# Kernel tuning notes

Measured on AMD Instinct MI355X. Metric: run time of the kernel, lower is better.

## Reference

```python
import jax, jax.numpy as jnp
import numpy as np

# --- batched state-vector quantum circuit sim: AngleEmbedding(RY) + BasicEntanglerLayers(RX + ring CNOT) ---

def _ry(state, theta, wire, n):
    # per-sample RY(theta) on `wire`; state: (B,) + (2,)*n complex
    ax = wire + 1
    c = jnp.cos(0.5 * theta).reshape((-1,) + (1,) * (n - 1)).astype(state.dtype)
    s = jnp.sin(0.5 * theta).reshape((-1,) + (1,) * (n - 1)).astype(state.dtype)
    s0 = jnp.take(state, 0, axis=ax)
    s1 = jnp.take(state, 1, axis=ax)
    return jnp.stack([c * s0 - s * s1, s * s0 + c * s1], axis=ax)

def _rx(state, theta, wire, n):
    # scalar RX(theta) on `wire` (shared weight across batch)
    ax = wire + 1
    c = jnp.cos(0.5 * theta).astype(state.dtype)
    s = (-1j * jnp.sin(0.5 * theta)).astype(state.dtype)
    s0 = jnp.take(state, 0, axis=ax)
    s1 = jnp.take(state, 1, axis=ax)
    return jnp.stack([c * s0 + s * s1, s * s0 + c * s1], axis=ax)

def _cnot(state, ctrl, tgt):
    ax_c = ctrl + 1
    s0 = jnp.take(state, 0, axis=ax_c)
    s1 = jnp.take(state, 1, axis=ax_c)
    ax_t = tgt + 1 if tgt < ctrl else tgt  # target axis index after removing ctrl axis
    s1 = jnp.flip(s1, axis=ax_t)
    return jnp.stack([s0, s1], axis=ax_c)

def _circuit(x_qin, qweights):
    # x_qin: (Bn, n) angles; qweights: (L, n)
    Bn, n = x_qin.shape
    state = jnp.zeros((Bn,) + (2,) * n, jnp.complex64)
    state = state.at[(slice(None),) + (0,) * n].set(1.0)
    for w in range(n):  # AngleEmbedding, rotation='Y'
        state = _ry(state, x_qin[:, w], w, n)
    for l in range(qweights.shape[0]):  # BasicEntanglerLayers
        for w in range(n):
            state = _rx(state, qweights[l, w], w, n)
        for w in range(n):
            state = _cnot(state, w, (w + 1) % n)
    probs = jnp.real(state * jnp.conj(state))
    outs = []
    for w in range(n):  # <Z_w> = P(bit_w=0) - P(bit_w=1)
        axes = tuple(a for a in range(1, n + 1) if a != w + 1)
        p = probs.sum(axis=axes)  # (Bn, 2)
        outs.append(p[:, 0] - p[:, 1])
    return jnp.stack(outs, axis=-1).astype(jnp.float32)


def setup_inputs() -> dict:
    key = jax.random.key(0)
    ks = jax.random.split(key, 9)
    B, N, H, NQ, L = 16, 1024, 256, 8, 2
    x = jax.random.normal(ks[0], (B, N, H), jnp.float32)
    norm_adj = jax.random.uniform(ks[1], (N, N), jnp.float32) / N
    Wg = jax.random.normal(ks[2], (H, H), jnp.float32) * 0.02
    bg = jax.random.normal(ks[3], (H,), jnp.float32) * 0.02
    Wpre = jax.random.normal(ks[4], (NQ, H), jnp.float32) * 0.05
    bpre = jax.random.normal(ks[5], (NQ,), jnp.float32) * 0.02
    qweights = jax.random.uniform(ks[6], (L, NQ), jnp.float32) * (2.0 * np.pi)
    Wpost = jax.random.normal(ks[7], (H, NQ), jnp.float32) * 0.1
    bpost = jax.random.normal(ks[8], (H,), jnp.float32) * 0.02
    return {"x": x, "norm_adj": norm_adj, "Wg": Wg, "bg": bg, "Wpre": Wpre,
            "bpre": bpre, "qweights": qweights, "Wpost": Wpost, "bpost": bpost}


def reference(x, norm_adj, Wg, bg, Wpre, bpre, qweights, Wpost, bpost):
    # GCN aggregation + GELU(Linear)  (dropout is identity in eval mode)
    x_agg = jnp.einsum('ij,bjh->bih', norm_adj, x)
    x_agg = jax.nn.gelu(x_agg @ Wg.T + bg, approximate=False)
    B, N, H = x_agg.shape
    x_flat = x_agg.reshape(B * N, H).astype(jnp.float32)
    x_qin = jnp.tanh(x_flat @ Wpre.T + bpre) * np.pi
    q_out = _circuit(x_qin, qweights)          # (B*N, n_qubits)
    out = (q_out @ Wpost.T + bpost).reshape(B, N, H)
    return out
```

## Files before the change

kernel.cpp:

```cpp
#include <hip/hip_runtime.h>
#include <math.h>

typedef __attribute__((ext_vector_type(8))) short bf16x8;
typedef _Float16 f16x8 __attribute__((ext_vector_type(8)));
typedef __attribute__((ext_vector_type(4))) float f32x4;

#define PI_F 3.14159265358979323846f

__device__ __forceinline__ unsigned short f2bf(float f) {
  unsigned int u = __float_as_uint(f);
  u += 0x7FFFu + ((u >> 16) & 1u);
  return (unsigned short)(u >> 16);
}

__device__ __forceinline__ float bf2f(unsigned short u) {
  return __uint_as_float(((unsigned int)u) << 16);
}

__device__ __forceinline__ void async_ld16(const unsigned short* g, unsigned short* l) {
  __builtin_amdgcn_global_load_lds(
      (const __attribute__((address_space(1))) void*)g,
      (__attribute__((address_space(3))) void*)l,
      16, 0, 0);
}

__device__ __forceinline__ float fast_erf(float x) {
  float a = fabsf(x);
  float t = 1.0f / fmaf(0.3275911f, a, 1.0f);
  float p = t * fmaf(t, fmaf(t, fmaf(t, fmaf(t, 1.061405429f, -1.453152027f),
                                     1.421413741f), -0.284496736f), 0.254829592f);
  float e = __expf(-a * a);
  float r = 1.0f - p * e;
  return copysignf(r, x);
}

__device__ __forceinline__ float fast_tanh(float a) {
  float e = __expf(2.0f * a);
  return 1.0f - 2.0f / (e + 1.0f);
}

template<int ML, int MR>
__device__ __forceinline__ void apply_rx(float re[4], float im[4], float c, float s) {
  float pr[4], pi[4];
  #pragma unroll
  for (int r = 0; r < 4; r++) {
    float vr = re[r ^ MR], vi = im[r ^ MR];
    if (ML) { vr = __shfl_xor(vr, ML, 64); vi = __shfl_xor(vi, ML, 64); }
    pr[r] = vr; pi[r] = vi;
  }
  #pragma unroll
  for (int r = 0; r < 4; r++) {
    re[r] = fmaf(c, re[r],  s * pi[r]);
    im[r] = fmaf(c, im[r], -s * pr[r]);
  }
}

__device__ __forceinline__ void fold_reduce8(float v[8], int L) {
  #pragma unroll
  for (int step = 0; step < 3; step++) {
    int d = 1 << step;
    int half = 4 >> step;
    bool hi = (L & d) != 0;
    #pragma unroll
    for (int w = 0; w < half; w++) {
      float send = hi ? v[w] : v[w + half];
      float recv = __shfl_xor(send, d, 64);
      v[w] = (hi ? v[w + half] : v[w]) + recv;
    }
  }
  v[0] += __shfl_xor(v[0], 8, 64);
  v[0] += __shfl_xor(v[0], 16, 64);
  v[0] += __shfl_xor(v[0], 32, 64);
}

__global__ __launch_bounds__(256)
void prep_kernel(const float* __restrict__ adj, unsigned short* __restrict__ adj_bf,
                 const float* __restrict__ Wg, unsigned short* __restrict__ Wg_bf,
                 const float* __restrict__ qw, unsigned short* __restrict__ Uri,
                 const float* __restrict__ Wpost, _Float16* __restrict__ Gt,
                 const float* __restrict__ x, unsigned short* __restrict__ xT) {
  __shared__ float smem[1056];
  int bid = blockIdx.x, t = threadIdx.x;
  if (bid < 1024) {
    int i = bid * 256 + t;
    float4 v = ((const float4*)adj)[i];
    ushort4 o; o.x = f2bf(v.x); o.y = f2bf(v.y); o.z = f2bf(v.z); o.w = f2bf(v.w);
    ((ushort4*)adj_bf)[i] = o;
  } else if (bid < 1088) {
    int i = (bid - 1024) * 256 + t;
    float4 v = ((const float4*)Wg)[i];
    ushort4 o; o.x = f2bf(v.x); o.y = f2bf(v.y); o.z = f2bf(v.z); o.w = f2bf(v.w);
    ((ushort4*)Wg_bf)[i] = o;
  } else if (bid < 1152) {
    if (t < 16) { smem[t] = cosf(0.5f * qw[t]); smem[16 + t] = sinf(0.5f * qw[t]); }
    __syncthreads();
    int wv = t >> 6, L = t & 63;
    int k = (bid - 1088) * 4 + wv;
    float re[4], im[4];
    #pragma unroll
    for (int r = 0; r < 4; r++) { re[r] = (r * 64 + L == k) ? 1.f : 0.f; im[r] = 0.f; }
    apply_rx<1, 0>(re, im, smem[0], smem[16]);
    apply_rx<2, 0>(re, im, smem[1], smem[17]);
    apply_rx<4, 0>(re, im, smem[2], smem[18]);
    apply_rx<8, 0>(re, im, smem[3], smem[19]);
    apply_rx<16, 0>(re, im, smem[4], smem[20]);
    apply_rx<32, 0>(re, im, smem[5], smem[21]);
    apply_rx<0, 1>(re, im, smem[6], smem[22]);
    apply_rx<0, 2>(re, im, smem[7], smem[23]);
    apply_rx<3, 0>(re, im, smem[8], smem[24]);
    apply_rx<6, 0>(re, im, smem[9], smem[25]);
    apply_rx<12, 0>(re, im, smem[10], smem[26]);
    apply_rx<24, 0>(re, im, smem[11], smem[27]);
    apply_rx<48, 0>(re, im, smem[12], smem[28]);
    apply_rx<32, 1>(re, im, smem[13], smem[29]);
    apply_rx<0, 3>(re, im, smem[14], smem[30]);
    apply_rx<3, 2>(re, im, smem[15], smem[31]);
    const int M[8] = {0xAB, 0xFD, 0xFA, 0xF5, 0xEA, 0xD5, 0xAA, 0x55};
    #pragma unroll
    for (int r = 0; r < 4; r++) {
      int n = 0;
      #pragma unroll
      for (int w = 0; w < 8; w++) {
        int bit = (__popc(L & (M[w] & 63)) ^ __popc((r << 6) & M[w])) & 1;
        n |= bit << w;
      }
      int row_re = ((n >> 4) << 5) + (n & 15);
      Uri[(size_t)row_re * 256 + k] = f2bf(re[r]);
      Uri[(size_t)(row_re + 16) * 256 + k] = f2bf(im[r]);
    }
  } else if (bid < 1168) {
    int tid = (bid - 1152) * 256 + t;
    int h = tid >> 4;
    int n0 = (tid & 15) << 4;
    float wv8[8];
    #pragma unroll
    for (int w = 0; w < 8; w++) wv8[w] = Wpost[h * 8 + w];
    #pragma unroll
    for (int j = 0; j < 16; j++) {
      int n = n0 + j;
      float sum = 0.f;
      #pragma unroll
      for (int w = 0; w < 8; w++) sum += ((n >> w) & 1) ? -wv8[w] : wv8[w];
      Gt[h * 256 + n] = (_Float16)sum;
    }
  } else {
    int tb = bid - 1168;
    int jt = tb & 31, ht = (tb >> 5) & 7, bb = tb >> 8;
    int tx = t & 31, ty = t >> 5;
    const float* xb = x + (size_t)bb * 1024 * 256;
    #pragma unroll
    for (int i = 0; i < 4; i++) {
      int j = jt * 32 + ty + i * 8;
      smem[(ty + i * 8) * 33 + tx] = xb[(size_t)j * 256 + ht * 32 + tx];
    }
    __syncthreads();
    unsigned short* xTb = xT + (size_t)bb * 256 * 1024;
    #pragma unroll
    for (int i = 0; i < 4; i++) {
      int h = ht * 32 + ty + i * 8;
      xTb[(size_t)h * 1024 + jt * 32 + tx] = f2bf(smem[tx * 33 + ty + i * 8]);
    }
  }
}

__global__ __launch_bounds__(256)
void gemm1_kernel(const unsigned short* __restrict__ A,
                  const unsigned short* __restrict__ Bt,
                  unsigned short* __restrict__ C,
                  int K, int tilesN, int ldC) {
  __shared__ unsigned short As[2 * 128 * 32];
  __shared__ unsigned short Bs[2 * 64 * 32];
  int rr  = blockIdx.x;
  int im  = rr / tilesN;
  int in_ = rr % tilesN;
  const unsigned short* Ab  = A  + (long long)im * 128 * K;
  const unsigned short* Btb = Bt + (long long)in_ * 64 * K;

  int t = threadIdx.x;
  int wv = t >> 6, lane = t & 63;
  int wm = wv >> 1, wn = wv & 1;
  int l15 = lane & 15, quad = lane >> 4;

  f32x4 acc[4][2] = {};

  for (int kk = 0; kk < K; kk += 64) {
    __syncthreads();
    #pragma unroll
    for (int kb = 0; kb < 2; kb++) {
      #pragma unroll
      for (int q = 0; q < 2; q++) {
        int ch = q * 256 + t;
        async_ld16(Ab + (long long)(ch >> 2) * K + kk + kb * 32 + (ch & 3) * 8,
                   &As[kb * 4096 + ch * 8]);
      }
      {
        int ch = t;
        async_ld16(Btb + (long long)(ch >> 2) * K + kk + kb * 32 + (ch & 3) * 8,
                   &Bs[kb * 2048 + ch * 8]);
      }
    }
    __syncthreads();
    #pragma unroll
    for (int kb = 0; kb < 2; kb++) {
      bf16x8 af[4], bfr[2];
      #pragma unroll
      for (int mt = 0; mt < 4; mt++)
        af[mt] = *(const bf16x8*)&As[kb * 4096 + (wm * 64 + mt * 16 + l15) * 32 + quad * 8];
      #pragma unroll
      for (int nt = 0; nt < 2; nt++)
        bfr[nt] = *(const bf16x8*)&Bs[kb * 2048 + (wn * 32 + nt * 16 + l15) * 32 + quad * 8];
      #pragma unroll
      for (int mt = 0; mt < 4; mt++)
        #pragma unroll
        for (int nt = 0; nt < 2; nt++)
          acc[mt][nt] = __builtin_amdgcn_mfma_f32_16x16x32_bf16(af[mt], bfr[nt], acc[mt][nt], 0, 0, 0);
    }
  }

  int n0 = in_ * 64;
  #pragma unroll
  for (int mt = 0; mt < 4; mt++) {
    #pragma unroll
    for (int nt = 0; nt < 2; nt++) {
      int colg = n0 + wn * 32 + nt * 16 + l15;
      #pragma unroll
      for (int r = 0; r < 4; r++) {
        int rowg = im * 128 + wm * 64 + mt * 16 + quad * 4 + r;
        C[(size_t)rowg * ldC + colg] = f2bf(acc[mt][nt][r]);
      }
    }
  }
}

__global__ __launch_bounds__(256)
void qfused_kernel(const unsigned short* __restrict__ xagg,
                   const unsigned short* __restrict__ Wg,
                   const float* __restrict__ bg,
                   const float* __restrict__ Wpre, const float* __restrict__ bpre,
                   const unsigned short* __restrict__ Uri,
                   const _Float16* __restrict__ Gt,
                   const float* __restrict__ bpost,
                   float* __restrict__ out) {
  __shared__ __align__(16) char smemraw[32768];
  unsigned short* gs  = (unsigned short*)smemraw;
  _Float16*       Ts  = (_Float16*)smemraw;
  unsigned short* P0s = (unsigned short*)(smemraw + 16384);

  int t = threadIdx.x;
  int wv = t >> 6, lane = t & 63;
  int l15 = lane & 15, quad = lane >> 4;

  const unsigned short* Ab = xagg + (size_t)blockIdx.x * 32 * 256;

  f32x4 acc[2][4] = {};
  {
    const unsigned short* Ap = Ab + (size_t)l15 * 256 + quad * 8;
    const unsigned short* Wp = Wg + (size_t)(wv * 64 + l15) * 256 + quad * 8;
    bf16x8 af[2][2], wf[2][4];
    #pragma unroll
    for (int mt = 0; mt < 2; mt++) af[0][mt] = *(const bf16x8*)(Ap + mt * 4096);
    #pragma unroll
    for (int nt = 0; nt < 4; nt++) wf[0][nt] = *(const bf16x8*)(Wp + nt * 4096);
    #pragma unroll
    for (int k8 = 0; k8 < 8; k8++) {
      int cur = k8 & 1, nxt = cur ^ 1;
      if (k8 < 7) {
        #pragma unroll
        for (int mt = 0; mt < 2; mt++)
          af[nxt][mt] = *(const bf16x8*)(Ap + (k8 + 1) * 32 + mt * 4096);
        #pragma unroll
        for (int nt = 0; nt < 4; nt++)
          wf[nxt][nt] = *(const bf16x8*)(Wp + (k8 + 1) * 32 + nt * 4096);
      }
      #pragma unroll
      for (int mt = 0; mt < 2; mt++)
        #pragma unroll
        for (int nt = 0; nt < 4; nt++)
          acc[mt][nt] = __builtin_amdgcn_mfma_f32_16x16x32_bf16(af[cur][mt], wf[cur][nt], acc[mt][nt], 0, 0, 0);
    }
  }
  #pragma unroll
  for (int mt = 0; mt < 2; mt++) {
    #pragma unroll
    for (int nt = 0; nt < 4; nt++) {
      int col = wv * 64 + nt * 16 + l15;
      float bgl = bg[col];
      #pragma unroll
      for (int r = 0; r < 4; r++) {
        int row = mt * 16 + quad * 4 + r;
        float v = acc[mt][nt][r] + bgl;
        v = 0.5f * v * (1.0f + fast_erf(v * 0.7071067811865475f));
        gs[row * 256 + col] = f2bf(v);
      }
    }
  }
  float4 wp[8];
  #pragma unroll
  for (int w = 0; w < 8; w++) wp[w] = *(const float4*)&Wpre[w * 256 + 4 * lane];
  float bprel = bpre[4 * (lane & 1) + (lane & 2) + ((lane >> 2) & 1)];
  __syncthreads();

  #pragma unroll
  for (int rr = 0; rr < 8; rr++) {
    int row = wv * 8 + rr;
    ushort4 gu = *(const ushort4*)&gs[row * 256 + 4 * lane];
    float g0 = bf2f(gu.x), g1 = bf2f(gu.y), g2 = bf2f(gu.z), g3 = bf2f(gu.w);
    float ang[8];
    #pragma unroll
    for (int w = 0; w < 8; w++) {
      float4 w4 = wp[w];
      float a = g0 * w4.x;
      a = fmaf(g1, w4.y, a);
      a = fmaf(g2, w4.z, a);
      a = fmaf(g3, w4.w, a);
      ang[w] = a;
    }
    fold_reduce8(ang, lane);
    float th = (0.5f * PI_F) * fast_tanh(ang[0] + bprel);
    float c = __cosf(th), s = __sinf(th);
    float cw[8], sw[8];
    #pragma unroll
    for (int w = 0; w < 8; w++) {
      int src = ((w >> 2) & 1) | (w & 2) | ((w & 1) << 2);
      cw[w] = __shfl(c, src, 64);
      sw[w] = __shfl(s, src, 64);
    }
    float pl = 1.f;
    #pragma unroll
    for (int b = 0; b < 6; b++) pl *= ((lane >> b) & 1) ? sw[b + 2] : cw[b + 2];
    ushort4 o;
    o.x = f2bf(pl * cw[0] * cw[1]);
    o.y = f2bf(pl * sw[0] * cw[1]);
    o.z = f2bf(pl * cw[0] * sw[1]);
    o.w = f2bf(pl * sw[0] * sw[1]);
    int j = lane & 7;
    int cswz = (j >> 1) ^ ((row >> 1) & 3);
    *(ushort4*)((char*)P0s + (lane >> 3) * 2048 + row * 64 + cswz * 16 + (j & 1) * 8) = o;
  }
  __syncthreads();

  f32x4 acc1[2][8] = {};
  {
    const unsigned short* Up = Uri + (size_t)(wv * 128 + l15) * 256 + quad * 8;
    const char* Pp = (const char*)P0s + l15 * 64 + (((quad ^ ((l15 >> 1) & 3))) << 4);
    bf16x8 pa[2][2], ua[2][8];
    #pragma unroll
    for (int mt = 0; mt < 2; mt++) pa[0][mt] = *(const bf16x8*)(Pp + mt * 1024);
    #pragma unroll
    for (int nt = 0; nt < 8; nt++) ua[0][nt] = *(const bf16x8*)(Up + nt * 4096);
    #pragma unroll
    for (int k8 = 0; k8 < 8; k8++) {
      int cur = k8 & 1, nxt = cur ^ 1;
      if (k8 < 7) {
        #pragma unroll
        for (int mt = 0; mt < 2; mt++)
          pa[nxt][mt] = *(const bf16x8*)(Pp + (k8 + 1) * 2048 + mt * 1024);
        #pragma unroll
        for (int nt = 0; nt < 8; nt++)
          ua[nxt][nt] = *(const bf16x8*)(Up + (k8 + 1) * 32 + nt * 4096);
      }
      #pragma unroll
      for (int mt = 0; mt < 2; mt++)
        #pragma unroll
        for (int nt = 0; nt < 8; nt++)
          acc1[mt][nt] = __builtin_amdgcn_mfma_f32_16x16x32_bf16(pa[cur][mt], ua[cur][nt], acc1[mt][nt], 0, 0, 0);
    }
  }

  #pragma unroll
  for (int mt = 0; mt < 2; mt++) {
    #pragma unroll
    for (int p = 0; p < 4; p++) {
      int kb = wv * 2 + (p >> 1);
      int cip = (p & 1) * 16 + l15;
      int ch = cip >> 3;
      #pragma unroll
      for (int r = 0; r < 4; r++) {
        int row = mt * 16 + quad * 4 + r;
        float tre = acc1[mt][2 * p][r], tim = acc1[mt][2 * p + 1][r];
        *(_Float16*)((char*)Ts + kb * 2048 + row * 64 +
                     ((ch ^ ((row >> 1) & 3)) << 4) + (cip & 7) * 2)
            = (_Float16)(tre * tre + tim * tim);
      }
    }
  }
  __syncthreads();

  f32x4 acc2[2][4] = {};
  {
    const _Float16* Gp = Gt + (size_t)(wv * 64 + l15) * 256 + quad * 8;
    const char* Tp = (const char*)Ts + l15 * 64 + (((quad ^ ((l15 >> 1) & 3))) << 4);
    f16x8 tf[2][2], gf[2][4];
    #pragma unroll
    for (int mt = 0; mt < 2; mt++) tf[0][mt] = *(const f16x8*)(Tp + mt * 1024);
    #pragma unroll
    for (int nt = 0; nt < 4; nt++) gf[0][nt] = *(const f16x8*)(Gp + nt * 4096);
    #pragma unroll
    for (int k8 = 0; k8 < 8; k8++) {
      int cur = k8 & 1, nxt = cur ^ 1;
      if (k8 < 7) {
        #pragma unroll
        for (int mt = 0; mt < 2; mt++)
          tf[nxt][mt] = *(const f16x8*)(Tp + (k8 + 1) * 2048 + mt * 1024);
        #pragma unroll
        for (int nt = 0; nt < 4; nt++)
          gf[nxt][nt] = *(const f16x8*)(Gp + (k8 + 1) * 32 + nt * 4096);
      }
      #pragma unroll
      for (int mt = 0; mt < 2; mt++)
        #pragma unroll
        for (int nt = 0; nt < 4; nt++)
          acc2[mt][nt] = __builtin_amdgcn_mfma_f32_16x16x32_f16(tf[cur][mt], gf[cur][nt], acc2[mt][nt], 0, 0, 0);
    }
  }

  #pragma unroll
  for (int mt = 0; mt < 2; mt++) {
    #pragma unroll
    for (int nt = 0; nt < 4; nt++) {
      int col = wv * 64 + nt * 16 + l15;
      float bp = bpost[col];
      #pragma unroll
      for (int r = 0; r < 4; r++) {
        int row = mt * 16 + quad * 4 + r;
        int s = blockIdx.x * 32 + row;
        int orow = (s & 15) * 1024 + (s >> 4);
        out[(size_t)orow * 256 + col] = acc2[mt][nt][r] + bp;
      }
    }
  }
}

extern "C" void kernel_launch(void* const* d_in, const int* in_sizes, int n_in,
                              void* d_out, int out_size, void* d_ws, size_t ws_size,
                              hipStream_t stream) {
  const float* x     = (const float*)d_in[0];
  const float* adj   = (const float*)d_in[1];
  const float* Wg    = (const float*)d_in[2];
  const float* bg    = (const float*)d_in[3];
  const float* Wpre  = (const float*)d_in[4];
  const float* bpre  = (const float*)d_in[5];
  const float* qw    = (const float*)d_in[6];
  const float* Wpost = (const float*)d_in[7];
  const float* bpost = (const float*)d_in[8];
  float* out = (float*)d_out;

  char* ws = (char*)d_ws;
  unsigned short* adj_bf  = (unsigned short*)(ws + 0);
  unsigned short* Wg_bf   = (unsigned short*)(ws + 2097152);
  unsigned short* xT_bf   = (unsigned short*)(ws + 2228224);
  unsigned short* xagg_bf = (unsigned short*)(ws + 10616832);
  unsigned short* Uri     = (unsigned short*)(ws + 19005440);
  _Float16*       Gt      = (_Float16*)(ws + 19267584);

  prep_kernel<<<5264, 256, 0, stream>>>(adj, adj_bf, Wg, Wg_bf, qw, Uri,
                                        Wpost, Gt, x, xT_bf);

  gemm1_kernel<<<512, 256, 0, stream>>>(adj_bf, xT_bf, xagg_bf, 1024, 64, 4096);

  qfused_kernel<<<512, 256, 0, stream>>>(xagg_bf, Wg_bf, bg, Wpre, bpre, Uri, Gt, bpost, out);
}
```

Measured before the change: 149.1 us.

## Shrink GEMM tiles, swizzle LDS, widen fused quantum kernel to 512 threads

The aggregation GEMM moves from 128x64 to 64x64 tiles, which doubles the grid to 1024 blocks, and adds an XOR swizzle to its LDS layout to avoid bank conflicts. The fused quantum kernel grows to 512 threads, so each wave covers half as many output columns. Its Wpre projection now runs on MFMA with a hi/lo bf16 split of the weights, and partial sums are reduced through shared memory instead of a shuffle fold. The register double-buffer prefetch is restructured to load two steps ahead, trading more parallelism and lower per-thread register pressure for extra syncs and more LDS.

```diff
diff --git a/kernel.cpp b/kernel.cpp
--- a/kernel.cpp
+++ b/kernel.cpp
@@ -53,24 +53,6 @@
     re[r] = fmaf(c, re[r],  s * pi[r]);
     im[r] = fmaf(c, im[r], -s * pr[r]);
   }
-}
-
-__device__ __forceinline__ void fold_reduce8(float v[8], int L) {
-  #pragma unroll
-  for (int step = 0; step < 3; step++) {
-    int d = 1 << step;
-    int half = 4 >> step;
-    bool hi = (L & d) != 0;
-    #pragma unroll
-    for (int w = 0; w < half; w++) {
-      float send = hi ? v[w] : v[w + half];
-      float recv = __shfl_xor(send, d, 64);
-      v[w] = (hi ? v[w + half] : v[w]) + recv;
-    }
-  }
-  v[0] += __shfl_xor(v[0], 8, 64);
-  v[0] += __shfl_xor(v[0], 16, 64);
-  v[0] += __shfl_xor(v[0], 32, 64);
 }
 
 __global__ __launch_bounds__(256)
@@ -168,12 +150,12 @@
                   const unsigned short* __restrict__ Bt,
                   unsigned short* __restrict__ C,
                   int K, int tilesN, int ldC) {
-  __shared__ unsigned short As[2 * 128 * 32];
+  __shared__ unsigned short As[2 * 64 * 32];
   __shared__ unsigned short Bs[2 * 64 * 32];
   int rr  = blockIdx.x;
   int im  = rr / tilesN;
   int in_ = rr % tilesN;
-  const unsigned short* Ab  = A  + (long long)im * 128 * K;
+  const unsigned short* Ab  = A  + (long long)im * 64 * K;
   const unsigned short* Btb = Bt + (long long)in_ * 64 * K;
 
   int t = threadIdx.x;
@@ -181,36 +163,35 @@
   int wm = wv >> 1, wn = wv & 1;
   int l15 = lane & 15, quad = lane >> 4;
 
-  f32x4 acc[4][2] = {};
+  int srow = t >> 2;
+  int skc  = (t & 3) ^ ((srow >> 1) & 3);
+  long long sgo = (long long)srow * K + skc * 8;
+
+  f32x4 acc[2][2] = {};
 
   for (int kk = 0; kk < K; kk += 64) {
     __syncthreads();
     #pragma unroll
     for (int kb = 0; kb < 2; kb++) {
-      #pragma unroll
-      for (int q = 0; q < 2; q++) {
-        int ch = q * 256 + t;
-        async_ld16(Ab + (long long)(ch >> 2) * K + kk + kb * 32 + (ch & 3) * 8,
-                   &As[kb * 4096 + ch * 8]);
-      }
-      {
-        int ch = t;
-        async_ld16(Btb + (long long)(ch >> 2) * K + kk + kb * 32 + (ch & 3) * 8,
-                   &Bs[kb * 2048 + ch * 8]);
-      }
+      async_ld16(Ab + sgo + kk + kb * 32, &As[kb * 2048 + t * 8]);
+      async_ld16(Btb + sgo + kk + kb * 32, &Bs[kb * 2048 + t * 8]);
     }
     __syncthreads();
     #pragma unroll
     for (int kb = 0; kb < 2; kb++) {
-      bf16x8 af[4], bfr[2];
-      #pragma unroll
-      for (int mt = 0; mt < 4; mt++)
-        af[mt] = *(const bf16x8*)&As[kb * 4096 + (wm * 64 + mt * 16 + l15) * 32 + quad * 8];
-      #pragma unroll
-      for (int nt = 0; nt < 2; nt++)
-        bfr[nt] = *(const bf16x8*)&Bs[kb * 2048 + (wn * 32 + nt * 16 + l15) * 32 + quad * 8];
-      #pragma unroll
-      for (int mt = 0; mt < 4; mt++)
+      bf16x8 af[2], bfr[2];
+      #pragma unroll
+      for (int mt = 0; mt < 2; mt++) {
+        int row = wm * 32 + mt * 16 + l15;
+        af[mt] = *(const bf16x8*)&As[kb * 2048 + row * 32 + ((quad ^ ((row >> 1) & 3)) * 8)];
+      }
+      #pragma unroll
+      for (int nt = 0; nt < 2; nt++) {
+        int row = wn * 32 + nt * 16 + l15;
+        bfr[nt] = *(const bf16x8*)&Bs[kb * 2048 + row * 32 + ((quad ^ ((row >> 1) & 3)) * 8)];
+      }
+      #pragma unroll
+      for (int mt = 0; mt < 2; mt++)
         #pragma unroll
         for (int nt = 0; nt < 2; nt++)
           acc[mt][nt] = __builtin_amdgcn_mfma_f32_16x16x32_bf16(af[mt], bfr[nt], acc[mt][nt], 0, 0, 0);
@@ -219,20 +200,20 @@
 
   int n0 = in_ * 64;
   #pragma unroll
-  for (int mt = 0; mt < 4; mt++) {
+  for (int mt = 0; mt < 2; mt++) {
     #pragma unroll
     for (int nt = 0; nt < 2; nt++) {
       int colg = n0 + wn * 32 + nt * 16 + l15;
       #pragma unroll
       for (int r = 0; r < 4; r++) {
-        int rowg = im * 128 + wm * 64 + mt * 16 + quad * 4 + r;
+        int rowg = im * 64 + wm * 32 + mt * 16 + quad * 4 + r;
         C[(size_t)rowg * ldC + colg] = f2bf(acc[mt][nt][r]);
       }
     }
   }
 }
 
-__global__ __launch_bounds__(256)
+__global__ __launch_bounds__(512, 4)
 void qfused_kernel(const unsigned short* __restrict__ xagg,
                    const unsigned short* __restrict__ Wg,
                    const float* __restrict__ bg,
@@ -241,10 +222,12 @@
                    const _Float16* __restrict__ Gt,
                    const float* __restrict__ bpost,
                    float* __restrict__ out) {
-  __shared__ __align__(16) char smemraw[32768];
+  __shared__ __align__(16) char smemraw[34816];
   unsigned short* gs  = (unsigned short*)smemraw;
   _Float16*       Ts  = (_Float16*)smemraw;
   unsigned short* P0s = (unsigned short*)(smemraw + 16384);
+  float*          prt = (float*)(smemraw + 16384);
+  float*          csw = (float*)(smemraw + 32768);
 
   int t = threadIdx.x;
   int wv = t >> 6, lane = t & 63;
@@ -252,79 +235,104 @@
 
   const unsigned short* Ab = xagg + (size_t)blockIdx.x * 32 * 256;
 
-  f32x4 acc[2][4] = {};
+  f32x4 acc[2][2] = {};
   {
     const unsigned short* Ap = Ab + (size_t)l15 * 256 + quad * 8;
-    const unsigned short* Wp = Wg + (size_t)(wv * 64 + l15) * 256 + quad * 8;
-    bf16x8 af[2][2], wf[2][4];
-    #pragma unroll
-    for (int mt = 0; mt < 2; mt++) af[0][mt] = *(const bf16x8*)(Ap + mt * 4096);
-    #pragma unroll
-    for (int nt = 0; nt < 4; nt++) wf[0][nt] = *(const bf16x8*)(Wp + nt * 4096);
+    const unsigned short* Wp = Wg + (size_t)(wv * 32 + l15) * 256 + quad * 8;
+    bf16x8 af[2][2], wf[2][2];
+    #pragma unroll
+    for (int sl = 0; sl < 2; sl++) {
+      #pragma unroll
+      for (int mt = 0; mt < 2; mt++) af[sl][mt] = *(const bf16x8*)(Ap + sl * 32 + mt * 4096);
+      #pragma unroll
+      for (int nt = 0; nt < 2; nt++) wf[sl][nt] = *(const bf16x8*)(Wp + sl * 32 + nt * 4096);
+    }
     #pragma unroll
     for (int k8 = 0; k8 < 8; k8++) {
-      int cur = k8 & 1, nxt = cur ^ 1;
-      if (k8 < 7) {
-        #pragma unroll
-        for (int mt = 0; mt < 2; mt++)
-          af[nxt][mt] = *(const bf16x8*)(Ap + (k8 + 1) * 32 + mt * 4096);
-        #pragma unroll
-        for (int nt = 0; nt < 4; nt++)
-          wf[nxt][nt] = *(const bf16x8*)(Wp + (k8 + 1) * 32 + nt * 4096);
-      }
+      int cur = k8 & 1;
       #pragma unroll
       for (int mt = 0; mt < 2; mt++)
         #pragma unroll
-        for (int nt = 0; nt < 4; nt++)
+        for (int nt = 0; nt < 2; nt++)
           acc[mt][nt] = __builtin_amdgcn_mfma_f32_16x16x32_bf16(af[cur][mt], wf[cur][nt], acc[mt][nt], 0, 0, 0);
+      if (k8 < 6) {
+        #pragma unroll
+        for (int mt = 0; mt < 2; mt++) af[cur][mt] = *(const bf16x8*)(Ap + (k8 + 2) * 32 + mt * 4096);
+        #pragma unroll
+        for (int nt = 0; nt < 2; nt++) wf[cur][nt] = *(const bf16x8*)(Wp + (k8 + 2) * 32 + nt * 4096);
+      }
     }
   }
   #pragma unroll
   for (int mt = 0; mt < 2; mt++) {
     #pragma unroll
-    for (int nt = 0; nt < 4; nt++) {
-      int col = wv * 64 + nt * 16 + l15;
+    for (int nt = 0; nt < 2; nt++) {
+      int col = wv * 32 + nt * 16 + l15;
       float bgl = bg[col];
+      int c = nt * 16 + l15, chunk = c >> 3, e = c & 7;
       #pragma unroll
       for (int r = 0; r < 4; r++) {
         int row = mt * 16 + quad * 4 + r;
         float v = acc[mt][nt][r] + bgl;
         v = 0.5f * v * (1.0f + fast_erf(v * 0.7071067811865475f));
-        gs[row * 256 + col] = f2bf(v);
-      }
-    }
-  }
-  float4 wp[8];
-  #pragma unroll
-  for (int w = 0; w < 8; w++) wp[w] = *(const float4*)&Wpre[w * 256 + 4 * lane];
-  float bprel = bpre[4 * (lane & 1) + (lane & 2) + ((lane >> 2) & 1)];
+        *(unsigned short*)((char*)gs + wv * 2048 + row * 64 +
+                           ((chunk ^ ((row >> 1) & 3)) << 4) + e * 2) = f2bf(v);
+      }
+    }
+  }
   __syncthreads();
 
-  #pragma unroll
-  for (int rr = 0; rr < 8; rr++) {
-    int row = wv * 8 + rr;
-    ushort4 gu = *(const ushort4*)&gs[row * 256 + 4 * lane];
-    float g0 = bf2f(gu.x), g1 = bf2f(gu.y), g2 = bf2f(gu.z), g3 = bf2f(gu.w);
-    float ang[8];
-    #pragma unroll
-    for (int w = 0; w < 8; w++) {
-      float4 w4 = wp[w];
-      float a = g0 * w4.x;
-      a = fmaf(g1, w4.y, a);
-      a = fmaf(g2, w4.z, a);
-      a = fmaf(g3, w4.w, a);
-      ang[w] = a;
-    }
-    fold_reduce8(ang, lane);
-    float th = (0.5f * PI_F) * fast_tanh(ang[0] + bprel);
-    float c = __cosf(th), s = __sinf(th);
-    float cw[8], sw[8];
-    #pragma unroll
-    for (int w = 0; w < 8; w++) {
-      int src = ((w >> 2) & 1) | (w & 2) | ((w & 1) << 2);
-      cw[w] = __shfl(c, src, 64);
-      sw[w] = __shfl(s, src, 64);
-    }
+  {
+    const float* wrow = Wpre + (size_t)(l15 & 7) * 256 + wv * 32 + quad * 8;
+    float4 wa = *(const float4*)wrow;
+    float4 wb = *(const float4*)(wrow + 4);
+    float v8[8] = {wa.x, wa.y, wa.z, wa.w, wb.x, wb.y, wb.z, wb.w};
+    bf16x8 whi, wlo;
+    #pragma unroll
+    for (int j = 0; j < 8; j++) {
+      unsigned short h = f2bf(v8[j]);
+      whi[j] = (short)h;
+      wlo[j] = (short)f2bf(v8[j] - bf2f(h));
+    }
+    const char* gp = (const char*)gs + wv * 2048;
+    f32x4 aacc[2] = {};
+    #pragma unroll
+    for (int mt = 0; mt < 2; mt++) {
+      int row = mt * 16 + l15;
+      bf16x8 ga = *(const bf16x8*)(gp + row * 64 + ((quad ^ ((row >> 1) & 3)) << 4));
+      aacc[mt] = __builtin_amdgcn_mfma_f32_16x16x32_bf16(ga, whi, aacc[mt], 0, 0, 0);
+      aacc[mt] = __builtin_amdgcn_mfma_f32_16x16x32_bf16(ga, wlo, aacc[mt], 0, 0, 0);
+    }
+    if (l15 < 8) {
+      #pragma unroll
+      for (int mt = 0; mt < 2; mt++)
+        #pragma unroll
+        for (int r = 0; r < 4; r++)
+          prt[wv * 256 + (mt * 16 + quad * 4 + r) * 8 + l15] = aacc[mt][r];
+    }
+  }
+  __syncthreads();
+
+  if (t < 256) {
+    float s = 0.f;
+    #pragma unroll
+    for (int k = 0; k < 8; k++) s += prt[k * 256 + t];
+    float th = (0.5f * PI_F) * fast_tanh(s + bpre[t & 7]);
+    int row = t >> 3, w = t & 7;
+    csw[row * 16 + w] = __cosf(th);
+    csw[row * 16 + 8 + w] = __sinf(th);
+  }
+  __syncthreads();
+
+  #pragma unroll
+  for (int rr = 0; rr < 4; rr++) {
+    int row = wv * 4 + rr;
+    float4 c0 = *(const float4*)&csw[row * 16];
+    float4 c1 = *(const float4*)&csw[row * 16 + 4];
+    float4 s0 = *(const float4*)&csw[row * 16 + 8];
+    float4 s1 = *(const float4*)&csw[row * 16 + 12];
+    float cw[8] = {c0.x, c0.y, c0.z, c0.w, c1.x, c1.y, c1.z, c1.w};
+    float sw[8] = {s0.x, s0.y, s0.z, s0.w, s1.x, s1.y, s1.z, s1.w};
     float pl = 1.f;
     #pragma unroll
     for (int b = 0; b < 6; b++) pl *= ((lane >> b) & 1) ? sw[b + 2] : cw[b + 2];
@@ -333,92 +341,92 @@
     o.y = f2bf(pl * sw[0] * cw[1]);
     o.z = f2bf(pl * cw[0] * sw[1]);
     o.w = f2bf(pl * sw[0] * sw[1]);
-    int j = lane & 7;
-    int cswz = (j >> 1) ^ ((row >> 1) & 3);
-    *(ushort4*)((char*)P0s + (lane >> 3) * 2048 + row * 64 + cswz * 16 + (j & 1) * 8) = o;
+    int jj = lane & 7;
+    int cswz = (jj >> 1) ^ ((row >> 1) & 3);
+    *(ushort4*)((char*)P0s + (lane >> 3) * 2048 + row * 64 + cswz * 16 + (jj & 1) * 8) = o;
   }
   __syncthreads();
 
-  f32x4 acc1[2][8] = {};
+  f32x4 acc1[2][4] = {};
   {
-    const unsigned short* Up = Uri + (size_t)(wv * 128 + l15) * 256 + quad * 8;
-    const char* Pp = (const char*)P0s + l15 * 64 + (((quad ^ ((l15 >> 1) & 3))) << 4);
-    bf16x8 pa[2][2], ua[2][8];
-    #pragma unroll
-    for (int mt = 0; mt < 2; mt++) pa[0][mt] = *(const bf16x8*)(Pp + mt * 1024);
-    #pragma unroll
-    for (int nt = 0; nt < 8; nt++) ua[0][nt] = *(const bf16x8*)(Up + nt * 4096);
+    const unsigned short* Up = Uri + (size_t)(wv * 64 + l15) * 256 + quad * 8;
+    const char* Pp = (const char*)P0s + l15 * 64 + ((quad ^ ((l15 >> 1) & 3)) << 4);
+    bf16x8 pa[2][2], ua[2][4];
+    #pragma unroll
+    for (int sl = 0; sl < 2; sl++) {
+      #pragma unroll
+      for (int mt = 0; mt < 2; mt++) pa[sl][mt] = *(const bf16x8*)(Pp + sl * 2048 + mt * 1024);
+      #pragma unroll
+      for (int nt = 0; nt < 4; nt++) ua[sl][nt] = *(const bf16x8*)(Up + sl * 32 + nt * 4096);
+    }
     #pragma unroll
     for (int k8 = 0; k8 < 8; k8++) {
-      int cur = k8 & 1, nxt = cur ^ 1;
-      if (k8 < 7) {
-        #pragma unroll
-        for (int mt = 0; mt < 2; mt++)
-          pa[nxt][mt] = *(const bf16x8*)(Pp + (k8 + 1) * 2048 + mt * 1024);
-        #pragma unroll
-        for (int nt = 0; nt < 8; nt++)
-          ua[nxt][nt] = *(const bf16x8*)(Up + (k8 + 1) * 32 + nt * 4096);
-      }
+      int cur = k8 & 1;
       #pragma unroll
       for (int mt = 0; mt < 2; mt++)
         #pragma unroll
-        for (int nt = 0; nt < 8; nt++)
+        for (int nt = 0; nt < 4; nt++)
           acc1[mt][nt] = __builtin_amdgcn_mfma_f32_16x16x32_bf16(pa[cur][mt], ua[cur][nt], acc1[mt][nt], 0, 0, 0);
+      if (k8 < 6) {
+        #pragma unroll
+        for (int mt = 0; mt < 2; mt++) pa[cur][mt] = *(const bf16x8*)(Pp + (k8 + 2) * 2048 + mt * 1024);
+        #pragma unroll
+        for (int nt = 0; nt < 4; nt++) ua[cur][nt] = *(const bf16x8*)(Up + (k8 + 2) * 32 + nt * 4096);
+      }
     }
   }
 
   #pragma unroll
   for (int mt = 0; mt < 2; mt++) {
     #pragma unroll
-    for (int p = 0; p < 4; p++) {
-      int kb = wv * 2 + (p >> 1);
-      int cip = (p & 1) * 16 + l15;
-      int ch = cip >> 3;
+    for (int p = 0; p < 2; p++) {
+      int c = p * 16 + l15, chunk = c >> 3, e = c & 7;
       #pragma unroll
       for (int r = 0; r < 4; r++) {
         int row = mt * 16 + quad * 4 + r;
         float tre = acc1[mt][2 * p][r], tim = acc1[mt][2 * p + 1][r];
-        *(_Float16*)((char*)Ts + kb * 2048 + row * 64 +
-                     ((ch ^ ((row >> 1) & 3)) << 4) + (cip & 7) * 2)
+        *(_Float16*)((char*)Ts + wv * 2048 + row * 64 +
+                     ((chunk ^ ((row >> 1) & 3)) << 4) + e * 2)
             = (_Float16)(tre * tre + tim * tim);
       }
     }
   }
   __syncthreads();
 
-  f32x4 acc2[2][4] = {};
+  f32x4 acc2[2][2] = {};
   {
-    const _Float16* Gp = Gt + (size_t)(wv * 64 + l15) * 256 + quad * 8;
-    const char* Tp = (const char*)Ts + l15 * 64 + (((quad ^ ((l15 >> 1) & 3))) << 4);
-    f16x8 tf[2][2], gf[2][4];
-    #pragma unroll
-    for (int mt = 0; mt < 2; mt++) tf[0][mt] = *(const f16x8*)(Tp + mt * 1024);
-    #pragma unroll
-    for (int nt = 0; nt < 4; nt++) gf[0][nt] = *(const f16x8*)(Gp + nt * 4096);
+    const _Float16* Gp = Gt + (size_t)(wv * 32 + l15) * 256 + quad * 8;
+    const char* Tp = (const char*)Ts + l15 * 64 + ((quad ^ ((l15 >> 1) & 3)) << 4);
+    f16x8 tf[2][2], gf[2][2];
+    #pragma unroll
+    for (int sl = 0; sl < 2; sl++) {
+      #pragma unroll
+      for (int mt = 0; mt < 2; mt++) tf[sl][mt] = *(const f16x8*)(Tp + sl * 2048 + mt * 1024);
+      #pragma unroll
+      for (int nt = 0; nt < 2; nt++) gf[sl][nt] = *(const f16x8*)(Gp + sl * 32 + nt * 4096);
+    }
     #pragma unroll
     for (int k8 = 0; k8 < 8; k8++) {
-      int cur = k8 & 1, nxt = cur ^ 1;
-      if (k8 < 7) {
-        #pragma unroll
-        for (int mt = 0; mt < 2; mt++)
-          tf[nxt][mt] = *(const f16x8*)(Tp + (k8 + 1) * 2048 + mt * 1024);
-        #pragma unroll
-        for (int nt = 0; nt < 4; nt++)
-          gf[nxt][nt] = *(const f16x8*)(Gp + (k8 + 1) * 32 + nt * 4096);
-      }
+      int cur = k8 & 1;
       #pragma unroll
       for (int mt = 0; mt < 2; mt++)
         #pragma unroll
-        for (int nt = 0; nt < 4; nt++)
+        for (int nt = 0; nt < 2; nt++)
           acc2[mt][nt] = __builtin_amdgcn_mfma_f32_16x16x32_f16(tf[cur][mt], gf[cur][nt], acc2[mt][nt], 0, 0, 0);
+      if (k8 < 6) {
+        #pragma unroll
+        for (int mt = 0; mt < 2; mt++) tf[cur][mt] = *(const f16x8*)(Tp + (k8 + 2) * 2048 + mt * 1024);
+        #pragma unroll
+        for (int nt = 0; nt < 2; nt++) gf[cur][nt] = *(const f16x8*)(Gp + (k8 + 2) * 32 + nt * 4096);
+      }
     }
   }
 
   #pragma unroll
   for (int mt = 0; mt < 2; mt++) {
     #pragma unroll
-    for (int nt = 0; nt < 4; nt++) {
-      int col = wv * 64 + nt * 16 + l15;
+    for (int nt = 0; nt < 2; nt++) {
+      int col = wv * 32 + nt * 16 + l15;
       float bp = bpost[col];
       #pragma unroll
       for (int r = 0; r < 4; r++) {
@@ -456,7 +464,7 @@
   prep_kernel<<<5264, 256, 0, stream>>>(adj, adj_bf, Wg, Wg_bf, qw, Uri,
                                         Wpost, Gt, x, xT_bf);
 
-  gemm1_kernel<<<512, 256, 0, stream>>>(adj_bf, xT_bf, xagg_bf, 1024, 64, 4096);
-
-  qfused_kernel<<<512, 256, 0, stream>>>(xagg_bf, Wg_bf, bg, Wpre, bpre, Uri, Gt, bpost, out);
-}
+  gemm1_kernel<<<1024, 256, 0, stream>>>(adj_bf, xT_bf, xagg_bf, 1024, 64, 4096);
+
+  qfused_kernel<<<512, 512, 0, stream>>>(xagg_bf, Wg_bf, bg, Wpre, bpre, Uri, Gt, bpost, out);
+}
```

Result: faster. 142.8 us (-4.2%).
